# Optimization experiments

Hardware: AMD Instinct MI355X
Metric: run time of the kernel (lower is better)

Reference implementation:

```python
import jax, jax.numpy as jnp
import numpy as np

H, D, K = 8, 512, 64
EPS = 1e-12


def _l2norm(x):
    # F.normalize(p=2, dim=-1): x / max(||x||_2, eps)
    n = jnp.sqrt(jnp.sum(x * x, axis=-1, keepdims=True))
    return x / jnp.maximum(n, EPS)


def setup_inputs() -> dict:
    key = jax.random.key(0)
    ks = jax.random.split(key, 8)
    S, B = 1024, 16
    scale = 1.0 / np.sqrt(D)
    return {
        "query": jax.random.normal(ks[0], (S, B, D), dtype=jnp.float32),
        "key": jax.random.normal(ks[1], (S, B, D), dtype=jnp.float32),
        "value": jax.random.normal(ks[2], (S, B, D), dtype=jnp.float32),
        # stacked per-head projection weights, torch Linear convention [out,in]
        "WQ": jax.random.uniform(ks[3], (H, K, D), jnp.float32, -scale, scale),
        "WK": jax.random.uniform(ks[4], (H, K, D), jnp.float32, -scale, scale),
        "WV": jax.random.uniform(ks[5], (H, K, D), jnp.float32, -scale, scale),
        "Wout": jax.random.uniform(ks[6], (D, H * K), jnp.float32,
                                   -1.0 / np.sqrt(H * K), 1.0 / np.sqrt(H * K)),
    }


def reference(query, key, value, WQ, WK, WV, Wout):
    temp = K ** 0.5
    # project all heads at once: [S,B,D] x [H,K,D] -> [B,H,S,K]
    wq = _l2norm(jnp.einsum("sbd,hkd->bhsk", query, WQ))
    wk = _l2norm(jnp.einsum("sbd,hkd->bhsk", key, WK))
    wv = _l2norm(jnp.einsum("sbd,hkd->bhsk", value, WV))
    # cosine-similarity attention scores [B,H,Sq,Sk]
    scores = jnp.einsum("bhsk,bhtk->bhst", wq, wk) / temp
    aff = jax.nn.softmax(scores, axis=-1)
    out = jnp.einsum("bhst,bhtk->bhsk", aff, wv)  # [B,H,S,K]
    # concat heads -> [S,B,H*K] (matches torch per-head concat on last dim)
    Sq, B = query.shape[0], query.shape[1]
    concat = out.transpose(2, 0, 1, 3).reshape(Sq, B, H * K)
    return concat @ Wout.T  # [S,B,D]
```

## Files before the change

kernel.cpp:

```cpp
#include <hip/hip_runtime.h>
#include <cstdint>
#include <cstddef>

typedef unsigned int u32;
typedef unsigned short u16;
typedef __attribute__((ext_vector_type(8))) short short8;
typedef __attribute__((ext_vector_type(4))) float f32x4;

#define S_LEN 1024
#define BATCH 16
#define NHEAD 8
#define DMODEL 512
#define KHD 64
#define NROW (S_LEN * BATCH)

__device__ __forceinline__ u16 f2bf(float f) {
    u32 u = __float_as_uint(f);
    return (u16)((u + 0x7fffu + ((u >> 16) & 1u)) >> 16);
}

__device__ __forceinline__ void gl_lds16(const void* g, void* l) {
    __builtin_amdgcn_global_load_lds(
        (const __attribute__((address_space(1))) void*)(uintptr_t)g,
        (__attribute__((address_space(3))) void*)(uintptr_t)l, 16, 0, 0);
}

__global__ __launch_bounds__(256) void wcvt_kernel(
    const float* __restrict__ WQ, const float* __restrict__ WK,
    const float* __restrict__ WV, const float* __restrict__ Wo,
    u16* __restrict__ dst)
{
    const int m = blockIdx.y;
    const float* __restrict__ src = (m == 0) ? WQ : (m == 1) ? WK : (m == 2) ? WV : Wo;
    const int idx = (blockIdx.x * 256 + threadIdx.x) * 4;
    const float4 v = *(const float4*)(src + idx);
    u16 r[4];
    r[0] = f2bf(v.x); r[1] = f2bf(v.y); r[2] = f2bf(v.z); r[3] = f2bf(v.w);
    *(uint2*)(dst + (size_t)m * DMODEL * DMODEL + idx) = *(uint2*)r;
}

__global__ __launch_bounds__(512, 6) void proj_kernel(
    const float* __restrict__ q, const float* __restrict__ k,
    const float* __restrict__ v, const u16* __restrict__ Wb,
    u16* __restrict__ outN)
{
    __shared__ __align__(16) float Alds[2][128 * 32];
    __shared__ __align__(16) u16   Blds[2][128 * 32];

    const int tid  = threadIdx.x;
    const int wave = tid >> 6;
    const int lane = tid & 63;
    const int m16  = lane & 15;
    const int quad = lane >> 4;
    const int wm   = wave >> 1;
    const int wn   = wave & 1;

    const int bid  = blockIdx.x;
    const bool isM1 = bid < 1024;
    int z, bx, by, bb;
    if (isM1) { z = bid >> 9; by = (bid >> 7) & 3; bx = bid & 127; bb = 0; }
    else { const int r = bid - 1024; z = 2; bb = r >> 5; by = (r >> 3) & 3; bx = r & 7; }

    const int row0 = bx * 128;
    const int n0   = by * 128;
    const float* __restrict__ A32 = isM1 ? (z ? k : q) : (v + (size_t)bb * DMODEL);
    const size_t astr = isM1 ? (size_t)DMODEL : (size_t)BATCH * DMODEL;
    const u16* __restrict__ B = Wb + (size_t)z * DMODEL * DMODEL;

    f32x4 acc[2][4] = {};

    const int ar  = lane >> 3, ac = lane & 7;
    const int alc = ac ^ ar;
    const int br  = lane >> 2, bc = lane & 3;
    const int blc = bc ^ (br & 3);

    auto stage = [&](int kt, int bufi) {
#pragma unroll
        for (int j = 0; j < 2; j++) {
            const int row = wave * 16 + j * 8 + ar;
            gl_lds16(A32 + (size_t)(row0 + row) * astr + kt + alc * 4,
                     &Alds[bufi][(wave * 16 + j * 8) * 32]);
        }
        {
            const int row = wave * 16 + br;
            gl_lds16(B + (size_t)(n0 + row) * DMODEL + kt + blc * 8,
                     &Blds[bufi][(wave * 16) * 32]);
        }
    };
    auto compute = [&](int bufi) {
        short8 af[2], bfr[4];
#pragma unroll
        for (int mt = 0; mt < 2; mt++) {
            const int row = wm * 32 + mt * 16 + m16;
            const int pc  = (quad << 1) ^ (m16 & 7);
            const float4 lo = *(const float4*)&Alds[bufi][row * 32 + pc * 4];
            const float4 hi = *(const float4*)&Alds[bufi][row * 32 + (pc ^ 1) * 4];
            u32 pkv[4];
            asm("v_cvt_pk_bf16_f32 %0, %1, %2" : "=v"(pkv[0]) : "v"(lo.x), "v"(lo.y));
            asm("v_cvt_pk_bf16_f32 %0, %1, %2" : "=v"(pkv[1]) : "v"(lo.z), "v"(lo.w));
            asm("v_cvt_pk_bf16_f32 %0, %1, %2" : "=v"(pkv[2]) : "v"(hi.x), "v"(hi.y));
            asm("v_cvt_pk_bf16_f32 %0, %1, %2" : "=v"(pkv[3]) : "v"(hi.z), "v"(hi.w));
            af[mt] = *(const short8*)pkv;
        }
#pragma unroll
        for (int nt = 0; nt < 4; nt++) {
            const int row = wn * 64 + nt * 16 + m16;
            const int pc  = quad ^ (m16 & 3);
            bfr[nt] = *(const short8*)&Blds[bufi][row * 32 + pc * 8];
        }
#pragma unroll
        for (int mt = 0; mt < 2; mt++)
#pragma unroll
            for (int nt = 0; nt < 4; nt++)
                acc[mt][nt] = __builtin_amdgcn_mfma_f32_16x16x32_bf16(af[mt], bfr[nt], acc[mt][nt], 0, 0, 0);
    };

    stage(0, 0);
    stage(32, 1);
    asm volatile("s_waitcnt vmcnt(3)" ::: "memory");
    __builtin_amdgcn_s_barrier();
    __builtin_amdgcn_sched_barrier(0);

#pragma unroll
    for (int t = 0; t < 16; t++) {
        compute(t & 1);
        if (t < 14) {
            __builtin_amdgcn_s_barrier();
            __builtin_amdgcn_sched_barrier(0);
            stage((t + 2) * 32, t & 1);
        }
        if (t < 15) {
            if (t < 14) asm volatile("s_waitcnt vmcnt(3)" ::: "memory");
            else        asm volatile("s_waitcnt vmcnt(0)" ::: "memory");
            __builtin_amdgcn_s_barrier();
            __builtin_amdgcn_sched_barrier(0);
        }
    }

    const int h = (n0 >> 6) + wn;
    u16* outZ = outN + (size_t)z * ((size_t)BATCH * NHEAD * S_LEN * KHD);
    if (isM1) {
#pragma unroll
        for (int mt = 0; mt < 2; mt++) {
#pragma unroll
            for (int r = 0; r < 4; r++) {
                float ss = 0.0f;
#pragma unroll
                for (int nt = 0; nt < 4; nt++) ss += acc[mt][nt][r] * acc[mt][nt][r];
                ss += __shfl_xor(ss, 1);
                ss += __shfl_xor(ss, 2);
                ss += __shfl_xor(ss, 4);
                ss += __shfl_xor(ss, 8);
                const float sc = 1.0f / fmaxf(sqrtf(ss), 1e-12f);
                const int i = row0 + wm * 32 + mt * 16 + quad * 4 + r;
                const int s = i >> 4, bq = i & 15;
                u16* op = outZ + (((size_t)bq * NHEAD + h) * S_LEN + s) * KHD;
#pragma unroll
                for (int nt = 0; nt < 4; nt++)
                    op[nt * 16 + m16] = f2bf(acc[mt][nt][r] * sc);
            }
        }
    } else {
#pragma unroll
        for (int mt = 0; mt < 2; mt++) {
            float scl[4];
#pragma unroll
            for (int r = 0; r < 4; r++) {
                float ss = 0.0f;
#pragma unroll
                for (int nt = 0; nt < 4; nt++) ss += acc[mt][nt][r] * acc[mt][nt][r];
                ss += __shfl_xor(ss, 1);
                ss += __shfl_xor(ss, 2);
                ss += __shfl_xor(ss, 4);
                ss += __shfl_xor(ss, 8);
                scl[r] = 1.0f / fmaxf(sqrtf(ss), 1e-12f);
            }
            const int sbase = row0 + wm * 32 + mt * 16 + quad * 4;
#pragma unroll
            for (int nt = 0; nt < 4; nt++) {
                const int vcol = nt * 16 + m16;
                uint2 pk;
                pk.x = (u32)f2bf(acc[mt][nt][0] * scl[0]) |
                       ((u32)f2bf(acc[mt][nt][1] * scl[1]) << 16);
                pk.y = (u32)f2bf(acc[mt][nt][2] * scl[2]) |
                       ((u32)f2bf(acc[mt][nt][3] * scl[3]) << 16);
                u16* dp = outZ + (((size_t)bb * NHEAD + h) * KHD + vcol) * S_LEN + sbase;
                *(uint2*)dp = pk;
            }
        }
    }
}

__global__ __launch_bounds__(512, 2) void gemm_out_kernel(
    const u16* __restrict__ Abf,
    const u16* __restrict__ Wb,
    float* __restrict__ outP)
{
    __shared__ __align__(16) u16 Alds[2][128 * 64];
    __shared__ __align__(16) u16 Blds[2][128 * 64];

    const int tid  = threadIdx.x;
    const int wave = tid >> 6;
    const int lane = tid & 63;
    const int m16  = lane & 15;
    const int quad = lane >> 4;
    const int wm   = wave >> 1;
    const int wn   = wave & 1;
    const int n0   = blockIdx.y * 128;
    const int row0 = blockIdx.x * 128;

    const int brow   = lane >> 3;
    const int bchunk = (lane & 7) ^ brow;

    f32x4 acc[2][4] = {};

    auto stage = [&](int kt, int b) {
        const int colc = kt + bchunk * 8;
        const int hh   = colc >> 6;
        const int kk   = colc & 63;
        u16* la = &Alds[b][(wave * 16) * 64];
#pragma unroll
        for (int j = 0; j < 2; j++) {
            const int i  = row0 + wave * 16 + j * 8 + brow;
            const int ss = i >> 4, bx = i & 15;
            gl_lds16(Abf + (((size_t)(bx * NHEAD + hh) * S_LEN + ss) * KHD + kk),
                     la + j * 8 * 64);
        }
        const u16* bp = Wb + (size_t)(n0 + wave * 16 + brow) * DMODEL + kt + bchunk * 8;
        u16* lb = &Blds[b][(wave * 16) * 64];
#pragma unroll
        for (int j = 0; j < 2; j++)
            gl_lds16(bp + (size_t)j * 8 * DMODEL, lb + j * 8 * 64);
    };
    auto compute = [&](int b) {
#pragma unroll
        for (int half = 0; half < 2; half++) {
            short8 af[2], bfr[4];
#pragma unroll
            for (int mt = 0; mt < 2; mt++)
                af[mt] = *(const short8*)&Alds[b][(wm * 32 + mt * 16 + m16) * 64 +
                                                  (((half << 2) + quad) ^ (m16 & 7)) * 8];
#pragma unroll
            for (int nt = 0; nt < 4; nt++)
                bfr[nt] = *(const short8*)&Blds[b][(wn * 64 + nt * 16 + m16) * 64 +
                                                   (((half << 2) + quad) ^ (m16 & 7)) * 8];
#pragma unroll
            for (int mt = 0; mt < 2; mt++)
#pragma unroll
                for (int nt = 0; nt < 4; nt++)
                    acc[mt][nt] = __builtin_amdgcn_mfma_f32_16x16x32_bf16(af[mt], bfr[nt], acc[mt][nt], 0, 0, 0);
        }
    };

    stage(0, 0);
    stage(64, 1);
    asm volatile("s_waitcnt vmcnt(4)" ::: "memory");
    __builtin_amdgcn_s_barrier();
    __builtin_amdgcn_sched_barrier(0);

#pragma unroll
    for (int t = 0; t < 8; t++) {
        compute(t & 1);
        if (t < 6) {
            __builtin_amdgcn_s_barrier();
            __builtin_amdgcn_sched_barrier(0);
            stage((t + 2) * 64, t & 1);
        }
        if (t < 7) {
            if (t < 6) asm volatile("s_waitcnt vmcnt(4)" ::: "memory");
            else       asm volatile("s_waitcnt vmcnt(0)" ::: "memory");
            __builtin_amdgcn_s_barrier();
            __builtin_amdgcn_sched_barrier(0);
        }
    }

#pragma unroll
    for (int mt = 0; mt < 2; mt++) {
#pragma unroll
        for (int r = 0; r < 4; r++) {
            const int i = row0 + wm * 32 + mt * 16 + quad * 4 + r;
            float* op = outP + (size_t)i * DMODEL + n0 + wn * 64;
#pragma unroll
            for (int nt = 0; nt < 4; nt++)
                op[nt * 16 + m16] = acc[mt][nt][r];
        }
    }
}

__global__ __launch_bounds__(256, 2) void attn_kernel(
    const u16* __restrict__ wq, const u16* __restrict__ wk, const u16* __restrict__ wvT,
    u16* __restrict__ Xout)
{
    __shared__ __align__(16) u16 Klds[2][64 * 64];
    __shared__ __align__(16) u16 Vlds[2][64 * 64];
    __shared__ __align__(16) u16 Plds[4][4][16 * 32];

    const int tid  = threadIdx.x;
    const int wave = tid >> 6;
    const int lane = tid & 63;
    const int m16  = lane & 15;
    const int quad = lane >> 4;
    const int bh   = blockIdx.x;
    const int qt   = blockIdx.y;

    const u16* Qb = wq  + (size_t)bh * S_LEN * KHD;
    const u16* Kb = wk  + (size_t)bh * S_LEN * KHD;
    const u16* Vb = wvT + (size_t)bh * KHD * S_LEN;

    const int qr0 = qt * 256 + wave * 64;
    short8 qf[4][2];
#pragma unroll
    for (int qb = 0; qb < 4; qb++) {
        qf[qb][0] = *(const short8*)(Qb + (size_t)(qr0 + qb * 16 + m16) * KHD + quad * 8);
        qf[qb][1] = *(const short8*)(Qb + (size_t)(qr0 + qb * 16 + m16) * KHD + 32 + quad * 8);
    }

    short8 ones;
#pragma unroll
    for (int j = 0; j < 8; j++) ones[j] = (short)0x3F80;

    f32x4 o[4][4] = {};
    f32x4 ls[4]   = {};
    const float C1 = 0.125f, C2 = 0.0078125f;

    const int srow   = lane >> 3;
    const int schunk = (lane & 7) ^ srow;
    const int r0     = wave * 8 + srow;
    const int pswz   = (m16 >> 1) & 3;

    gl_lds16(Kb + (size_t)r0 * KHD + schunk * 8,               &Klds[0][(wave * 8) * 64]);
    gl_lds16(Kb + (size_t)(r0 + 32) * KHD + schunk * 8,        &Klds[0][(wave * 8 + 32) * 64]);
    gl_lds16(Vb + (size_t)r0 * S_LEN + schunk * 8,             &Vlds[0][(wave * 8) * 64]);
    gl_lds16(Vb + (size_t)(r0 + 32) * S_LEN + schunk * 8,      &Vlds[0][(wave * 8 + 32) * 64]);
    __syncthreads();

    for (int it = 0; it < S_LEN / 64; it++) {
        const int cur = it & 1;

        if (it + 1 < S_LEN / 64) {
            const int nxt = cur ^ 1;
            const int kt0 = (it + 1) * 64;
            gl_lds16(Kb + (size_t)(kt0 + r0) * KHD + schunk * 8,        &Klds[nxt][(wave * 8) * 64]);
            gl_lds16(Kb + (size_t)(kt0 + r0 + 32) * KHD + schunk * 8,   &Klds[nxt][(wave * 8 + 32) * 64]);
            gl_lds16(Vb + (size_t)r0 * S_LEN + kt0 + schunk * 8,        &Vlds[nxt][(wave * 8) * 64]);
            gl_lds16(Vb + (size_t)(r0 + 32) * S_LEN + kt0 + schunk * 8, &Vlds[nxt][(wave * 8 + 32) * 64]);
        }

#pragma unroll
        for (int cc = 0; cc < 2; cc++) {
#pragma unroll
            for (int mm = 0; mm < 2; mm++) {
                const int mt = cc * 2 + mm;
                const short8 kf0 = *(const short8*)&Klds[cur][(mt * 16 + m16) * 64 + (quad ^ (m16 & 7)) * 8];
                const short8 kf1 = *(const short8*)&Klds[cur][(mt * 16 + m16) * 64 + ((4 + quad) ^ (m16 & 7)) * 8];
#pragma unroll
                for (int qb = 0; qb < 4; qb++) {
                    f32x4 s = {};
                    s = __builtin_amdgcn_mfma_f32_16x16x32_bf16(kf0, qf[qb][0], s, 0, 0, 0);
                    s = __builtin_amdgcn_mfma_f32_16x16x32_bf16(kf1, qf[qb][1], s, 0, 0, 0);
                    u32 up[4];
#pragma unroll
                    for (int r = 0; r < 4; r++) {
                        const float y = s[r];
                        const float p = fmaf(fmaf(C2, y, C1), y, 1.0f);
                        up[r] = __float_as_uint(p);
                    }
                    uint2 pk;
                    pk.x = __builtin_amdgcn_perm(up[1], up[0], 0x07060302u);
                    pk.y = __builtin_amdgcn_perm(up[3], up[2], 0x07060302u);
                    *(uint2*)((char*)&Plds[wave][qb][0] + m16 * 64 +
                              ((((mm << 1) + (quad >> 1)) ^ pswz) << 4) + ((quad & 1) << 3)) = pk;
                }
            }

            short8 vfr[4];
#pragma unroll
            for (int vt = 0; vt < 4; vt++)
                vfr[vt] = *(const short8*)&Vlds[cur][(vt * 16 + m16) * 64 +
                                                     (((cc << 2) + quad) ^ (m16 & 7)) * 8];
            __builtin_amdgcn_s_setprio(1);
#pragma unroll
            for (int qb = 0; qb < 4; qb++) {
                const short8 pb = *(const short8*)((const char*)&Plds[wave][qb][0] + m16 * 64 +
                                                   ((quad ^ pswz) << 4));
                ls[qb] = __builtin_amdgcn_mfma_f32_16x16x32_bf16(ones, pb, ls[qb], 0, 0, 0);
#pragma unroll
                for (int vt = 0; vt < 4; vt++)
                    o[qb][vt] = __builtin_amdgcn_mfma_f32_16x16x32_bf16(vfr[vt], pb, o[qb][vt], 0, 0, 0);
            }
            __builtin_amdgcn_s_setprio(0);
        }

        __syncthreads();
    }

    u16* outB = Xout + (size_t)bh * S_LEN * KHD;
#pragma unroll
    for (int qb = 0; qb < 4; qb++) {
        const float inv = 1.0f / ls[qb][0];
        const int qrow = qr0 + qb * 16 + m16;
        u16* cp = outB + (size_t)qrow * KHD;
#pragma unroll
        for (int vt = 0; vt < 4; vt++) {
            uint2 pk;
            pk.x = (u32)f2bf(o[qb][vt][0] * inv) | ((u32)f2bf(o[qb][vt][1] * inv) << 16);
            pk.y = (u32)f2bf(o[qb][vt][2] * inv) | ((u32)f2bf(o[qb][vt][3] * inv) << 16);
            *(uint2*)(cp + vt * 16 + quad * 4) = pk;
        }
    }
}

extern "C" void kernel_launch(void* const* d_in, const int* in_sizes, int n_in,
                              void* d_out, int out_size, void* d_ws, size_t ws_size,
                              hipStream_t stream) {
    const float* q    = (const float*)d_in[0];
    const float* k    = (const float*)d_in[1];
    const float* v    = (const float*)d_in[2];
    const float* WQ   = (const float*)d_in[3];
    const float* WK   = (const float*)d_in[4];
    const float* WV   = (const float*)d_in[5];
    const float* Wout = (const float*)d_in[6];
    float* out = (float*)d_out;

    const size_t per = (size_t)BATCH * NHEAD * S_LEN * KHD;
    u16* wsQKV = (u16*)d_ws;
    u16* wsW   = wsQKV + 3 * per;

    wcvt_kernel<<<dim3(256, 4), 256, 0, stream>>>(WQ, WK, WV, Wout, wsW);

    proj_kernel<<<dim3(1536), 512, 0, stream>>>(q, k, v, wsW, wsQKV);

    attn_kernel<<<dim3(BATCH * NHEAD, S_LEN / 256), 256, 0, stream>>>(
        wsQKV, wsQKV + per, wsQKV + 2 * per, wsQKV);

    gemm_out_kernel<<<dim3(NROW / 128, DMODEL / 128), 512, 0, stream>>>(
        wsQKV, wsW + (size_t)3 * DMODEL * DMODEL, out);
}
```

Baseline: 243.7 us.

## Convert activations to bf16 at LDS write and double K-tile depth

```diff
diff --git a/kernel.cpp b/kernel.cpp
--- a/kernel.cpp
+++ b/kernel.cpp
@@ -39,13 +39,13 @@
     *(uint2*)(dst + (size_t)m * DMODEL * DMODEL + idx) = *(uint2*)r;
 }
 
-__global__ __launch_bounds__(512, 6) void proj_kernel(
+__global__ __launch_bounds__(512, 4) void proj_kernel(
     const float* __restrict__ q, const float* __restrict__ k,
     const float* __restrict__ v, const u16* __restrict__ Wb,
     u16* __restrict__ outN)
 {
-    __shared__ __align__(16) float Alds[2][128 * 32];
-    __shared__ __align__(16) u16   Blds[2][128 * 32];
+    __shared__ __align__(16) u16 Alds[2][128 * 64];
+    __shared__ __align__(16) u16 Blds[2][128 * 64];
 
     const int tid  = threadIdx.x;
     const int wave = tid >> 6;
@@ -69,73 +69,97 @@
 
     f32x4 acc[2][4] = {};
 
-    const int ar  = lane >> 3, ac = lane & 7;
-    const int alc = ac ^ ar;
-    const int br  = lane >> 2, bc = lane & 3;
-    const int blc = bc ^ (br & 3);
-
-    auto stage = [&](int kt, int bufi) {
-#pragma unroll
-        for (int j = 0; j < 2; j++) {
-            const int row = wave * 16 + j * 8 + ar;
-            gl_lds16(A32 + (size_t)(row0 + row) * astr + kt + alc * 4,
-                     &Alds[bufi][(wave * 16 + j * 8) * 32]);
-        }
-        {
-            const int row = wave * 16 + br;
-            gl_lds16(B + (size_t)(n0 + row) * DMODEL + kt + blc * 8,
-                     &Blds[bufi][(wave * 16) * 32]);
+    const int arow = wave * 16 + (lane >> 2);
+    const int ac0  = lane & 3;
+    const float* __restrict__ aPtr = A32 + (size_t)(row0 + arow) * astr;
+    const int brow   = lane >> 3;
+    const int bchunk = (lane & 7) ^ brow;
+
+    float4 pA[4], pB[4];
+
+#define LOADA(kt, rg)                                                           \
+    {                                                                           \
+        _Pragma("unroll")                                                       \
+        for (int j = 0; j < 4; j++)                                             \
+            rg[j] = *(const float4*)(aPtr + (kt) + (ac0 + 4 * j) * 4);          \
+    }
+#define WRITEA(rg, bufi)                                                        \
+    {                                                                           \
+        _Pragma("unroll")                                                       \
+        for (int j = 0; j < 4; j++) {                                           \
+            const int c = ac0 + 4 * j;                                          \
+            u32 lo, hi;                                                         \
+            asm("v_cvt_pk_bf16_f32 %0, %1, %2" : "=v"(lo) : "v"(rg[j].x), "v"(rg[j].y)); \
+            asm("v_cvt_pk_bf16_f32 %0, %1, %2" : "=v"(hi) : "v"(rg[j].z), "v"(rg[j].w)); \
+            uint2 pk; pk.x = lo; pk.y = hi;                                     \
+            *(uint2*)&Alds[bufi][arow * 64 + (((c >> 1) ^ (arow & 7)) << 3) +   \
+                                 ((c & 1) << 2)] = pk;                          \
+        }                                                                       \
+    }
+#define STAGEB(kt, bufi)                                                        \
+    {                                                                           \
+        const u16* bp = B + (size_t)(n0 + wave * 16 + brow) * DMODEL + (kt) +   \
+                        bchunk * 8;                                             \
+        u16* lb = &Blds[bufi][(wave * 16) * 64];                                \
+        gl_lds16(bp, lb);                                                       \
+        gl_lds16(bp + (size_t)8 * DMODEL, lb + 8 * 64);                         \
+    }
+
+    auto compute = [&](int bufi) {
+#pragma unroll
+        for (int half = 0; half < 2; half++) {
+            short8 af[2], bfr[4];
+#pragma unroll
+            for (int mt = 0; mt < 2; mt++)
+                af[mt] = *(const short8*)&Alds[bufi][(wm * 32 + mt * 16 + m16) * 64 +
+                                                     (((half << 2) + quad) ^ (m16 & 7)) * 8];
+#pragma unroll
+            for (int nt = 0; nt < 4; nt++)
+                bfr[nt] = *(const short8*)&Blds[bufi][(wn * 64 + nt * 16 + m16) * 64 +
+                                                      (((half << 2) + quad) ^ (m16 & 7)) * 8];
+#pragma unroll
+            for (int mt = 0; mt < 2; mt++)
+#pragma unroll
+                for (int nt = 0; nt < 4; nt++)
+                    acc[mt][nt] = __builtin_amdgcn_mfma_f32_16x16x32_bf16(af[mt], bfr[nt], acc[mt][nt], 0, 0, 0);
         }
     };
-    auto compute = [&](int bufi) {
-        short8 af[2], bfr[4];
-#pragma unroll
-        for (int mt = 0; mt < 2; mt++) {
-            const int row = wm * 32 + mt * 16 + m16;
-            const int pc  = (quad << 1) ^ (m16 & 7);
-            const float4 lo = *(const float4*)&Alds[bufi][row * 32 + pc * 4];
-            const float4 hi = *(const float4*)&Alds[bufi][row * 32 + (pc ^ 1) * 4];
-            u32 pkv[4];
-            asm("v_cvt_pk_bf16_f32 %0, %1, %2" : "=v"(pkv[0]) : "v"(lo.x), "v"(lo.y));
-            asm("v_cvt_pk_bf16_f32 %0, %1, %2" : "=v"(pkv[1]) : "v"(lo.z), "v"(lo.w));
-            asm("v_cvt_pk_bf16_f32 %0, %1, %2" : "=v"(pkv[2]) : "v"(hi.x), "v"(hi.y));
-            asm("v_cvt_pk_bf16_f32 %0, %1, %2" : "=v"(pkv[3]) : "v"(hi.z), "v"(hi.w));
-            af[mt] = *(const short8*)pkv;
-        }
-#pragma unroll
-        for (int nt = 0; nt < 4; nt++) {
-            const int row = wn * 64 + nt * 16 + m16;
-            const int pc  = quad ^ (m16 & 3);
-            bfr[nt] = *(const short8*)&Blds[bufi][row * 32 + pc * 8];
-        }
-#pragma unroll
-        for (int mt = 0; mt < 2; mt++)
-#pragma unroll
-            for (int nt = 0; nt < 4; nt++)
-                acc[mt][nt] = __builtin_amdgcn_mfma_f32_16x16x32_bf16(af[mt], bfr[nt], acc[mt][nt], 0, 0, 0);
-    };
-
-    stage(0, 0);
-    stage(32, 1);
-    asm volatile("s_waitcnt vmcnt(3)" ::: "memory");
+
+    LOADA(0, pA)
+    STAGEB(0, 0)
+    LOADA(64, pB)
+    STAGEB(64, 1)
+    asm volatile("s_waitcnt vmcnt(6)" ::: "memory");
+    __builtin_amdgcn_sched_barrier(0);
+    WRITEA(pA, 0)
+    asm volatile("s_waitcnt lgkmcnt(0)" ::: "memory");
     __builtin_amdgcn_s_barrier();
     __builtin_amdgcn_sched_barrier(0);
 
 #pragma unroll
-    for (int t = 0; t < 16; t++) {
+    for (int t = 0; t < 8; t++) {
         compute(t & 1);
-        if (t < 14) {
+        if (t < 6) {
             __builtin_amdgcn_s_barrier();
             __builtin_amdgcn_sched_barrier(0);
-            stage((t + 2) * 32, t & 1);
-        }
-        if (t < 15) {
-            if (t < 14) asm volatile("s_waitcnt vmcnt(3)" ::: "memory");
-            else        asm volatile("s_waitcnt vmcnt(0)" ::: "memory");
+            if (t & 1) { LOADA((t + 2) * 64, pB) }
+            else       { LOADA((t + 2) * 64, pA) }
+            STAGEB((t + 2) * 64, t & 1);
+        }
+        if (t < 7) {
+            if (t < 6) asm volatile("s_waitcnt vmcnt(6)" ::: "memory");
+            else       asm volatile("s_waitcnt vmcnt(0)" ::: "memory");
+            __builtin_amdgcn_sched_barrier(0);
+            if ((t + 1) & 1) { WRITEA(pB, 1) }
+            else             { WRITEA(pA, 0) }
+            asm volatile("s_waitcnt lgkmcnt(0)" ::: "memory");
             __builtin_amdgcn_s_barrier();
             __builtin_amdgcn_sched_barrier(0);
         }
     }
+#undef LOADA
+#undef WRITEA
+#undef STAGEB
 
     const int h = (n0 >> 6) + wn;
     u16* outZ = outN + (size_t)z * ((size_t)BATCH * NHEAD * S_LEN * KHD);
```

Result: no change. 241.4 us (-0.9%).
